# Performance work log

Measured on AMD Instinct MI355X. Metric: run time of the kernel, lower is better.

## Reference

```python
import jax, jax.numpy as jnp
import numpy as np

B, L, H, HEADS = 2, 2048, 1024, 16
D = H // HEADS  # head_dim = 64


def _rel_pos_bias(q, pos_emb):
    """Skewing trick: q is (b,h,L,d) (already scaled), pos_emb is (2L-1,d).
    Returns relative positional bias of shape (b,h,L,L)."""
    b, h, l, _ = q.shape
    p = jnp.einsum('bhid,jd->bhij', q, pos_emb)          # (b,h,L,2L-1)
    p = jnp.pad(p, ((0, 0), (0, 0), (0, 0), (0, 1)))     # (b,h,L,2L)
    p = p.reshape(b, h, l * 2 * l)                        # flatten last two dims
    p = jnp.pad(p, ((0, 0), (0, 0), (0, l - 1)))          # append L-1 zeros
    p = p.reshape(b, h, l + 1, 2 * l - 1)
    return p[:, :, :-1, -l:]                              # (b,h,L,L)


def setup_inputs() -> dict:
    key = jax.random.key(0)
    ks = jax.random.split(key, 12)
    s = 1.0 / np.sqrt(H)
    inp = {
        'query': jax.random.normal(ks[0], (B, L, H), jnp.float32),
        'key':   jax.random.normal(ks[1], (B, L, H), jnp.float32),
        'value': jax.random.normal(ks[2], (B, L, H), jnp.float32),
        'Wq_w': jax.random.normal(ks[3], (H, H), jnp.float32) * s,
        'Wq_b': jnp.zeros((H,), jnp.float32),
        'Wk_w': jax.random.normal(ks[4], (H, H), jnp.float32) * s,
        'Wk_b': jnp.zeros((H,), jnp.float32),
        'Wv_w': jax.random.normal(ks[5], (H, H), jnp.float32) * s,
        'Wv_b': jnp.zeros((H,), jnp.float32),
        'Wo_w': jax.random.normal(ks[6], (H, H), jnp.float32) * s,
        'Wo_b': jnp.zeros((H,), jnp.float32),
        'pos_emb': jax.random.normal(ks[7], (2 * L - 1, D), jnp.float32),
    }
    return inp


def reference(query, key, value, Wq_w, Wq_b, Wk_w, Wk_b, Wv_w, Wv_b, Wo_w, Wo_b, pos_emb):
    b = query.shape[0]
    q = query @ Wq_w.T + Wq_b
    k = key @ Wk_w.T + Wk_b
    v = value @ Wv_w.T + Wv_b
    # (b,L,h*d) -> (b,h,L,d)
    split = lambda x: x.reshape(b, L, HEADS, D).transpose(0, 2, 1, 3)
    q, k, v = split(q), split(k), split(v)
    q = q / np.sqrt(D)  # note: scaled q is also used for positional bias (faithful)
    attn = jnp.einsum('bhid,bhjd->bhij', q, k)
    attn = attn + _rel_pos_bias(q, pos_emb)
    causal = jnp.triu(jnp.full((L, L), -jnp.inf, jnp.float32), k=1)
    attn = attn + causal  # broadcasts over (b,h)
    score = jax.nn.softmax(attn, axis=-1)
    out = jnp.einsum('bhqk,bhkd->bhqd', score, v)
    out = out.transpose(0, 2, 1, 3).reshape(b, L, H)
    return out @ Wo_w.T + Wo_b
```

## Files before the change

### kernel.cpp

```cpp
#include <hip/hip_runtime.h>

#define L_SEQ 2048
#define NH    16
#define HD    64
#define HDIM  1024

typedef __attribute__((ext_vector_type(8))) short  short8;
typedef __attribute__((ext_vector_type(4))) float  f32x4;

__device__ __forceinline__ unsigned short f2bf(float f) {
    unsigned int u = __float_as_uint(f);
    u += 0x7fffu + ((u >> 16) & 1u);
    return (unsigned short)(u >> 16);
}

__device__ __forceinline__ short8 ld8(const unsigned short* p) {
    return *(const short8*)p;
}

__device__ __forceinline__ unsigned int cvtpk(float a, float b) {
    unsigned int r;
    asm("v_cvt_pk_bf16_f32 %0, %1, %2" : "=v"(r) : "v"(a), "v"(b));
    return r;
}

__device__ __forceinline__ void gl16(const unsigned short* g, unsigned short* l) {
    __builtin_amdgcn_global_load_lds(
        (const __attribute__((address_space(1))) void*)g,
        (__attribute__((address_space(3))) void*)l, 16, 0, 0);
}

__global__ __launch_bounds__(256) void cvt_x_kernel(const float* __restrict__ src,
                                                    unsigned short* __restrict__ dst) {
    const int i = blockIdx.x * 256 + threadIdx.x;
    const float4 a = ((const float4*)src)[2 * i];
    const float4 b = ((const float4*)src)[2 * i + 1];
    union { short8 v; unsigned int u[4]; } o;
    o.u[0] = cvtpk(a.x, a.y); o.u[1] = cvtpk(a.z, a.w);
    o.u[2] = cvtpk(b.x, b.y); o.u[3] = cvtpk(b.z, b.w);
    ((short8*)dst)[i] = o.v;
}

__global__ __launch_bounds__(256) void cvt_wpe_kernel(
    const float* __restrict__ Wq, const float* __restrict__ Wk,
    const float* __restrict__ Wv, const float* __restrict__ Wo,
    const float* __restrict__ pe,
    unsigned short* __restrict__ D, unsigned short* __restrict__ E) {
    const int y = blockIdx.y;
    const float* src = (y == 0) ? Wq : (y == 1) ? Wk : (y == 2) ? Wv : (y == 3) ? Wo : pe;
    unsigned short* dst = (y < 4) ? (D + (size_t)y * 1048576) : E;
    const int n8 = (y < 4) ? 131072 : 32760;
    const int i = blockIdx.x * 256 + threadIdx.x;
    if (i >= n8) return;
    const float4 a = ((const float4*)src)[2 * i];
    const float4 b = ((const float4*)src)[2 * i + 1];
    union { short8 v; unsigned int u[4]; } o;
    o.u[0] = cvtpk(a.x, a.y); o.u[1] = cvtpk(a.z, a.w);
    o.u[2] = cvtpk(b.x, b.y); o.u[3] = cvtpk(b.z, b.w);
    ((short8*)dst)[i] = o.v;
}

__device__ __forceinline__ void gemm_bf16_core(
    const unsigned short* __restrict__ Xb,
    const unsigned short* __restrict__ Wb,
    int row0, int col0,
    unsigned short* As, unsigned short* Bs,
    f32x4 (&acc)[4][4])
{
    const int t    = threadIdx.x;
    const int lane = t & 63;
    const int wid  = t >> 6;
    const int lr   = lane & 15;
    const int lg   = lane >> 4;
    const int wr   = (wid >> 1) << 6;
    const int wc   = (wid & 1) << 6;

    const int grow = lane >> 3;
    const int gcol = ((lane & 7) ^ grow) << 3;

#pragma unroll
    for (int m = 0; m < 4; ++m)
#pragma unroll
        for (int n = 0; n < 4; ++n)
            acc[m][n] = (f32x4)0.0f;

    const unsigned short* xs = Xb + (size_t)(row0 + grow) * 1024 + gcol;
    const unsigned short* ws = Wb + (size_t)(col0 + grow) * 1024 + gcol;

    for (int k0 = 0; k0 < 1024; k0 += 64) {
        __syncthreads();
#pragma unroll
        for (int i = 0; i < 4; ++i) {
            const int seg = (i << 2) + wid;
            gl16(xs + (size_t)(seg << 3) * 1024 + k0, As + seg * 512);
            gl16(ws + (size_t)(seg << 3) * 1024 + k0, Bs + seg * 512);
        }
        __syncthreads();

        short8 af[4][2], bf[4][2];
#pragma unroll
        for (int m = 0; m < 4; ++m) {
            const int row = wr + (m << 4) + lr;
#pragma unroll
            for (int h = 0; h < 2; ++h)
                af[m][h] = ld8(&As[row * 64 + ((((h << 2) + lg) ^ (lr & 7)) << 3)]);
        }
#pragma unroll
        for (int n = 0; n < 4; ++n) {
            const int row = wc + (n << 4) + lr;
#pragma unroll
            for (int h = 0; h < 2; ++h)
                bf[n][h] = ld8(&Bs[row * 64 + ((((h << 2) + lg) ^ (lr & 7)) << 3)]);
        }
#pragma unroll
        for (int m = 0; m < 4; ++m)
#pragma unroll
            for (int n = 0; n < 4; ++n) {
                acc[m][n] = __builtin_amdgcn_mfma_f32_16x16x32_bf16(af[m][0], bf[n][0], acc[m][n], 0, 0, 0);
                acc[m][n] = __builtin_amdgcn_mfma_f32_16x16x32_bf16(af[m][1], bf[n][1], acc[m][n], 0, 0, 0);
            }
    }
}

template<int MODE>
__global__ __launch_bounds__(256) void proj_kernel(
    const unsigned short* __restrict__ Xb, const unsigned short* __restrict__ Wb,
    const float* __restrict__ bias, unsigned short* __restrict__ out)
{
    __shared__ __align__(16) unsigned short As[128 * 64];
    __shared__ __align__(16) unsigned short Bs[128 * 64];

    const int d = blockIdx.x;
    const int y = ((d >> 6) << 3) | (d & 7);
    const int x = (d >> 3) & 7;
    const int row0 = y << 7, col0 = x << 7;

    f32x4 acc[4][4];
    gemm_bf16_core(Xb, Wb, row0, col0, As, Bs, acc);

    const int t = threadIdx.x;
    const int lane = t & 63;
    const int wid  = t >> 6;
    const int lr = lane & 15, lg = lane >> 4;
    const int wr = (wid >> 1) << 6, wc = (wid & 1) << 6;

    if (MODE <= 1) {
        const float scale = (MODE == 0) ? 0.125f : 1.0f;
#pragma unroll
        for (int n = 0; n < 4; ++n) {
            const int o = col0 + wc + (n << 4) + lr;
            const float bo = bias[o];
            const int h = o >> 6, dd = o & 63;
#pragma unroll
            for (int m = 0; m < 4; ++m) {
                const int ib = row0 + wr + (m << 4) + (lg << 2);
#pragma unroll
                for (int r = 0; r < 4; ++r) {
                    const int i = ib + r;
                    out[(((size_t)((i >> 11) * NH + h)) * L_SEQ + (i & (L_SEQ - 1))) * HD + dd] =
                        f2bf((acc[m][n][r] + bo) * scale);
                }
            }
        }
    } else {
#pragma unroll
        for (int n = 0; n < 4; ++n) {
            const int o = col0 + wc + (n << 4) + lr;
            const float bo = bias[o];
            const int h = o >> 6, dd = o & 63;
#pragma unroll
            for (int m = 0; m < 4; ++m) {
                const int ib = row0 + wr + (m << 4) + (lg << 2);
                const int b = ib >> 11, il = ib & (L_SEQ - 1);
                ushort4 pk;
                pk.x = f2bf(acc[m][n][0] + bo);
                pk.y = f2bf(acc[m][n][1] + bo);
                pk.z = f2bf(acc[m][n][2] + bo);
                pk.w = f2bf(acc[m][n][3] + bo);
                *(ushort4*)&out[(((size_t)(b * NH + h)) * HD + dd) * L_SEQ + il] = pk;
            }
        }
    }
}

__global__ __launch_bounds__(256) void outproj_kernel(
    const unsigned short* __restrict__ Ob, const unsigned short* __restrict__ Wb,
    const float* __restrict__ bias, float* __restrict__ Yout)
{
    __shared__ __align__(16) unsigned short As[128 * 64];
    __shared__ __align__(16) unsigned short Bs[128 * 64];

    const int d = blockIdx.x;
    const int y = ((d >> 6) << 3) | (d & 7);
    const int x = (d >> 3) & 7;
    const int row0 = y << 7, col0 = x << 7;

    f32x4 acc[4][4];
    gemm_bf16_core(Ob, Wb, row0, col0, As, Bs, acc);

    const int t = threadIdx.x;
    const int lane = t & 63;
    const int wid  = t >> 6;
    const int lr = lane & 15, lg = lane >> 4;
    const int wr = (wid >> 1) << 6, wc = (wid & 1) << 6;

#pragma unroll
    for (int n = 0; n < 4; ++n) {
        const int o = col0 + wc + (n << 4) + lr;
        const float bo = bias[o];
#pragma unroll
        for (int m = 0; m < 4; ++m) {
            const int ib = row0 + wr + (m << 4) + (lg << 2);
#pragma unroll
            for (int r = 0; r < 4; ++r)
                Yout[(size_t)(ib + r) * HDIM + o] = acc[m][n][r] + bo;
        }
    }
}

__global__ __launch_bounds__(256, 3) void attn_kernel(
    const unsigned short* __restrict__ Q,
    const unsigned short* __restrict__ Kt,
    const unsigned short* __restrict__ VT,
    const unsigned short* __restrict__ PE,
    unsigned short* __restrict__ O)
{
    __shared__ __align__(16) unsigned short Ks[2][64][64];
    __shared__ __align__(16) unsigned short Vs[2][64][64];
    __shared__ __align__(16) float blds_all[4][64][20];

    const int t    = threadIdx.x;
    const int wid  = t >> 6;
    const int lane = t & 63;
    const int lr   = lane & 15;
    const int lg   = lane >> 4;
    const int lk   = lg << 3;

    const int p   = blockIdx.x;
    const int bh  = p & 31;
    const int rb  = 31 - (p >> 5);
    const int i0  = rb << 6;
    const int i0w = i0 + (wid << 4);
    const int nt  = rb + 1;

    const unsigned short* kbase = Kt + (size_t)bh * L_SEQ * HD;
    const unsigned short* vbase = VT + (size_t)bh * HD * L_SEQ;

    const int srow = t >> 2;
    const int sc2  = (t & 3) << 1;
    const int swz  = srow & 7;

    short8 kstg[2], vstg[2];

    float (*blds)[20] = blds_all[wid];

    const unsigned short* qb = Q + ((size_t)bh * L_SEQ + i0w + lr) * HD + lk;
    const short8 aq0 = ld8(qb);
    const short8 aq1 = ld8(qb + 32);

    const int gi    = i0w + lr;
    const int idx0  = ((lg & 1) << 7) + (lr << 2);
    const int idx1  = idx0 + 64;
    const int selhi = lg >> 1;

    f32x4 oacc[4];
#pragma unroll
    for (int dt = 0; dt < 4; ++dt) oacc[dt] = (f32x4)0.0f;
    float mrun = -__builtin_inff();
    float lrun = 0.0f;

    const int jend = i0w + 15;

    f32x4 pqc = (f32x4)0.0f;
    {
        const unsigned short* pp = PE + (size_t)(2032 - i0w + lr) * HD + lk;
        pqc = __builtin_amdgcn_mfma_f32_16x16x32_bf16(aq0, ld8(pp), pqc, 0, 0, 0);
        pqc = __builtin_amdgcn_mfma_f32_16x16x32_bf16(aq1, ld8(pp + 32), pqc, 0, 0, 0);
    }

#pragma unroll
    for (int s = 0; s < 2; ++s) {
        kstg[s] = ld8(kbase + (size_t)srow * HD + ((sc2 + s) << 3));
        vstg[s] = ld8(vbase + (size_t)srow * L_SEQ + ((sc2 + s) << 3));
    }
#pragma unroll
    for (int s = 0; s < 2; ++s) {
        *(short8*)&Ks[0][srow][((sc2 + s) ^ swz) << 3] = kstg[s];
        *(short8*)&Vs[0][srow][((sc2 + s) ^ swz) << 3] = vstg[s];
    }
    __syncthreads();

    int cur = 0;
    for (int tt = 0; tt < nt; ++tt) {
        const int j0   = tt << 6;
        const bool more = (tt + 1 < nt);

        if (more) {
            const int jn = j0 + 64;
#pragma unroll
            for (int s = 0; s < 2; ++s) {
                kstg[s] = ld8(kbase + (size_t)(jn + srow) * HD + ((sc2 + s) << 3));
                vstg[s] = ld8(vbase + (size_t)srow * L_SEQ + jn + ((sc2 + s) << 3));
            }
        }

        if (j0 <= jend) {
            f32x4 s2[4];
#pragma unroll
            for (int ct = 0; ct < 4; ++ct) {
                const int row = (ct << 4) + lr;
                const short8 k0 = *(const short8*)&Ks[cur][row][(lg ^ (lr & 7)) << 3];
                const short8 k1 = *(const short8*)&Ks[cur][row][((4 + lg) ^ (lr & 7)) << 3];
                f32x4 a = (f32x4)0.0f;
                a = __builtin_amdgcn_mfma_f32_16x16x32_bf16(k0, aq0, a, 0, 0, 0);
                a = __builtin_amdgcn_mfma_f32_16x16x32_bf16(k1, aq1, a, 0, 0, 0);
                s2[ct] = a;
            }

            const int mlo = 2032 + j0 - i0w;
            f32x4 pq[5];
            pq[0] = pqc;
#pragma unroll
            for (int pt = 1; pt < 5; ++pt) {
                f32x4 a = (f32x4)0.0f;
                const unsigned short* pp = PE + (size_t)(mlo + (pt << 4) + lr) * HD + lk;
                a = __builtin_amdgcn_mfma_f32_16x16x32_bf16(aq0, ld8(pp), a, 0, 0, 0);
                a = __builtin_amdgcn_mfma_f32_16x16x32_bf16(aq1, ld8(pp + 32), a, 0, 0, 0);
                pq[pt] = a;
            }
            pqc = pq[4];

#pragma unroll
            for (int r = 0; r < 4; ++r) {
                const int qw = (lg << 2) + r;
                {
                    const int kr = lr + qw - 15;
                    if (kr >= 0) blds[kr][qw] = pq[0][r];
                }
#pragma unroll
                for (int pt = 1; pt < 4; ++pt)
                    blds[(pt << 4) + lr + qw - 15][qw] = pq[pt][r];
                {
                    const int kr = 49 + lr + qw;
                    if (kr < 64) blds[kr][qw] = pq[4][r];
                }
            }

#pragma unroll
            for (int ct = 0; ct < 4; ++ct)
#pragma unroll
                for (int r = 0; r < 4; ++r) {
                    const int krl = (ct << 4) + (lg << 2) + r;
                    const float v = s2[ct][r] + blds[krl][lr];
                    s2[ct][r] = (j0 + krl > gi) ? -__builtin_inff() : v;
                }

            float c0 = fmaxf(fmaxf(s2[0][0], s2[0][1]), fmaxf(s2[0][2], s2[0][3]));
            float c1 = fmaxf(fmaxf(s2[1][0], s2[1][1]), fmaxf(s2[1][2], s2[1][3]));
            float c2 = fmaxf(fmaxf(s2[2][0], s2[2][1]), fmaxf(s2[2][2], s2[2][3]));
            float c3 = fmaxf(fmaxf(s2[3][0], s2[3][1]), fmaxf(s2[3][2], s2[3][3]));
            float vmax = fmaxf(fmaxf(c0, c1), fmaxf(c2, c3));
            vmax = fmaxf(vmax, __shfl_xor(vmax, 16));
            vmax = fmaxf(vmax, __shfl_xor(vmax, 32));
            const float mnew = fmaxf(mrun, vmax);
            const float sc = __expf(mrun - mnew);
            mrun = mnew;
#pragma unroll
            for (int ct = 0; ct < 4; ++ct)
#pragma unroll
                for (int r = 0; r < 4; ++r)
                    s2[ct][r] = __expf(s2[ct][r] - mnew);
            float t0 = (s2[0][0] + s2[0][1]) + (s2[0][2] + s2[0][3]);
            float t1 = (s2[1][0] + s2[1][1]) + (s2[1][2] + s2[1][3]);
            float t2 = (s2[2][0] + s2[2][1]) + (s2[2][2] + s2[2][3]);
            float t3 = (s2[3][0] + s2[3][1]) + (s2[3][2] + s2[3][3]);
            float sum = (t0 + t1) + (t2 + t3);
            sum += __shfl_xor(sum, 16);
            sum += __shfl_xor(sum, 32);
            lrun = lrun * sc + sum;
#pragma unroll
            for (int dt = 0; dt < 4; ++dt)
#pragma unroll
                for (int r = 0; r < 4; ++r)
                    oacc[dt][r] *= sc;

            unsigned int pkl[4], pkh[4];
#pragma unroll
            for (int ct = 0; ct < 4; ++ct) {
                pkl[ct] = cvtpk(s2[ct][0], s2[ct][1]);
                pkh[ct] = cvtpk(s2[ct][2], s2[ct][3]);
            }
            union { short8 v; int u[4]; } pf0, pf1;
#pragma unroll
            for (int m = 0; m < 4; ++m) {
                const int bidx = (m & 2) ? idx1 : idx0;
                const int a0 = __builtin_amdgcn_ds_bpermute(bidx, (int)((m & 1) ? pkh[0] : pkl[0]));
                const int a1 = __builtin_amdgcn_ds_bpermute(bidx, (int)((m & 1) ? pkh[1] : pkl[1]));
                pf0.u[m] = selhi ? a1 : a0;
                const int b0 = __builtin_amdgcn_ds_bpermute(bidx, (int)((m & 1) ? pkh[2] : pkl[2]));
                const int b1 = __builtin_amdgcn_ds_bpermute(bidx, (int)((m & 1) ? pkh[3] : pkl[3]));
                pf1.u[m] = selhi ? b1 : b0;
            }

#pragma unroll
            for (int dt = 0; dt < 4; ++dt) {
                const int row = (dt << 4) + lr;
                const short8 v0 = *(const short8*)&Vs[cur][row][(lg ^ (lr & 7)) << 3];
                const short8 v1 = *(const short8*)&Vs[cur][row][((4 + lg) ^ (lr & 7)) << 3];
                oacc[dt] = __builtin_amdgcn_mfma_f32_16x16x32_bf16(v0, pf0.v, oacc[dt], 0, 0, 0);
                oacc[dt] = __builtin_amdgcn_mfma_f32_16x16x32_bf16(v1, pf1.v, oacc[dt], 0, 0, 0);
            }
        }

        if (more) {
#pragma unroll
            for (int s = 0; s < 2; ++s) {
                *(short8*)&Ks[cur ^ 1][srow][((sc2 + s) ^ swz) << 3] = kstg[s];
                *(short8*)&Vs[cur ^ 1][srow][((sc2 + s) ^ swz) << 3] = vstg[s];
            }
        }
        __syncthreads();
        cur ^= 1;
    }

    const float inv = 1.0f / lrun;
    const int b = bh >> 4, h = bh & 15;
#pragma unroll
    for (int dt = 0; dt < 4; ++dt) {
        uint2 u;
        u.x = cvtpk(oacc[dt][0] * inv, oacc[dt][1] * inv);
        u.y = cvtpk(oacc[dt][2] * inv, oacc[dt][3] * inv);
        *(uint2*)&O[((size_t)b * L_SEQ + i0w + lr) * HDIM + (h << 6) + (dt << 4) + (lg << 2)] = u;
    }
}

extern "C" void kernel_launch(void* const* d_in, const int* in_sizes, int n_in,
                              void* d_out, int out_size, void* d_ws, size_t ws_size,
                              hipStream_t stream) {
    (void)in_sizes; (void)n_in; (void)out_size;

    const float* query   = (const float*)d_in[0];
    const float* key_    = (const float*)d_in[1];
    const float* value   = (const float*)d_in[2];
    const float* Wq_w    = (const float*)d_in[3];
    const float* Wq_b    = (const float*)d_in[4];
    const float* Wk_w    = (const float*)d_in[5];
    const float* Wk_b    = (const float*)d_in[6];
    const float* Wv_w    = (const float*)d_in[7];
    const float* Wv_b    = (const float*)d_in[8];
    const float* Wo_w    = (const float*)d_in[9];
    const float* Wo_b    = (const float*)d_in[10];
    const float* pos_emb = (const float*)d_in[11];

    char* ws = (char*)d_ws;
    const size_t MB = 1024 * 1024;
    unsigned short* S1 = (unsigned short*)(ws);
    unsigned short* Qb = (unsigned short*)(ws + 8  * MB);
    unsigned short* Kb = (unsigned short*)(ws + 16 * MB);
    unsigned short* Vb = (unsigned short*)(ws + 24 * MB);
    unsigned short* D  = (unsigned short*)(ws + 32 * MB);
    unsigned short* E  = (unsigned short*)(ws + 40 * MB);

    const int npe = (2 * L_SEQ - 1) * HD;
    if (ws_size < (size_t)40 * MB + (size_t)npe * 2) return;

    cvt_wpe_kernel<<<dim3(512, 5), 256, 0, stream>>>(Wq_w, Wk_w, Wv_w, Wo_w, pos_emb, D, E);
    cvt_x_kernel<<<2048, 256, 0, stream>>>(query, S1);
    cvt_x_kernel<<<2048, 256, 0, stream>>>(key_, Vb);
    proj_kernel<0><<<256, 256, 0, stream>>>(S1, D, Wq_b, Qb);
    proj_kernel<1><<<256, 256, 0, stream>>>(Vb, D + 1048576, Wk_b, Kb);
    cvt_x_kernel<<<2048, 256, 0, stream>>>(value, S1);
    proj_kernel<2><<<256, 256, 0, stream>>>(S1, D + 2097152, Wv_b, Vb);
    attn_kernel<<<1024, 256, 0, stream>>>(Qb, Kb, Vb, E, S1);
    outproj_kernel<<<256, 256, 0, stream>>>(S1, D + 3145728, Wo_b, (float*)d_out);
}
```

Before: 203.1 us.

## Merge conversion and Q/K projection launches; stage K/V via direct global-to-LDS loads

```diff
diff --git a/kernel.cpp b/kernel.cpp
--- a/kernel.cpp
+++ b/kernel.cpp
@@ -28,6 +28,35 @@
     __builtin_amdgcn_global_load_lds(
         (const __attribute__((address_space(1))) void*)g,
         (__attribute__((address_space(3))) void*)l, 16, 0, 0);
+}
+
+__global__ __launch_bounds__(256) void cvt_a_kernel(
+    const float* __restrict__ q, const float* __restrict__ k,
+    const float* __restrict__ Wq, const float* __restrict__ Wk,
+    const float* __restrict__ Wv, const float* __restrict__ Wo,
+    const float* __restrict__ pe,
+    unsigned short* __restrict__ S1, unsigned short* __restrict__ Vb,
+    unsigned short* __restrict__ D, unsigned short* __restrict__ E)
+{
+    const int y = blockIdx.y;
+    const float* src; unsigned short* dst; int n8;
+    switch (y) {
+        case 0:  src = q;  dst = S1;            n8 = 524288; break;
+        case 1:  src = k;  dst = Vb;            n8 = 524288; break;
+        case 2:  src = Wq; dst = D;             n8 = 131072; break;
+        case 3:  src = Wk; dst = D + 1048576;   n8 = 131072; break;
+        case 4:  src = Wv; dst = D + 2097152;   n8 = 131072; break;
+        case 5:  src = Wo; dst = D + 3145728;   n8 = 131072; break;
+        default: src = pe; dst = E;             n8 = 32760;  break;
+    }
+    const int i = blockIdx.x * 256 + threadIdx.x;
+    if (i >= n8) return;
+    const float4 a = ((const float4*)src)[2 * i];
+    const float4 b = ((const float4*)src)[2 * i + 1];
+    union { short8 v; unsigned int u[4]; } o;
+    o.u[0] = cvtpk(a.x, a.y); o.u[1] = cvtpk(a.z, a.w);
+    o.u[2] = cvtpk(b.x, b.y); o.u[3] = cvtpk(b.z, b.w);
+    ((short8*)dst)[i] = o.v;
 }
 
 __global__ __launch_bounds__(256) void cvt_x_kernel(const float* __restrict__ src,
@@ -41,25 +70,6 @@
     ((short8*)dst)[i] = o.v;
 }
 
-__global__ __launch_bounds__(256) void cvt_wpe_kernel(
-    const float* __restrict__ Wq, const float* __restrict__ Wk,
-    const float* __restrict__ Wv, const float* __restrict__ Wo,
-    const float* __restrict__ pe,
-    unsigned short* __restrict__ D, unsigned short* __restrict__ E) {
-    const int y = blockIdx.y;
-    const float* src = (y == 0) ? Wq : (y == 1) ? Wk : (y == 2) ? Wv : (y == 3) ? Wo : pe;
-    unsigned short* dst = (y < 4) ? (D + (size_t)y * 1048576) : E;
-    const int n8 = (y < 4) ? 131072 : 32760;
-    const int i = blockIdx.x * 256 + threadIdx.x;
-    if (i >= n8) return;
-    const float4 a = ((const float4*)src)[2 * i];
-    const float4 b = ((const float4*)src)[2 * i + 1];
-    union { short8 v; unsigned int u[4]; } o;
-    o.u[0] = cvtpk(a.x, a.y); o.u[1] = cvtpk(a.z, a.w);
-    o.u[2] = cvtpk(b.x, b.y); o.u[3] = cvtpk(b.z, b.w);
-    ((short8*)dst)[i] = o.v;
-}
-
 __device__ __forceinline__ void gemm_bf16_core(
     const unsigned short* __restrict__ Xb,
     const unsigned short* __restrict__ Wb,
@@ -122,18 +132,26 @@
     }
 }
 
-template<int MODE>
-__global__ __launch_bounds__(256) void proj_kernel(
-    const unsigned short* __restrict__ Xb, const unsigned short* __restrict__ Wb,
-    const float* __restrict__ bias, unsigned short* __restrict__ out)
+__global__ __launch_bounds__(256) void proj_qk_kernel(
+    const unsigned short* __restrict__ Xq, const unsigned short* __restrict__ Xk,
+    const unsigned short* __restrict__ D,
+    const float* __restrict__ bq, const float* __restrict__ bk,
+    unsigned short* __restrict__ Qb, unsigned short* __restrict__ Kb)
 {
     __shared__ __align__(16) unsigned short As[128 * 64];
     __shared__ __align__(16) unsigned short Bs[128 * 64];
 
-    const int d = blockIdx.x;
+    const int z = blockIdx.x >> 8;
+    const int d = blockIdx.x & 255;
     const int y = ((d >> 6) << 3) | (d & 7);
     const int x = (d >> 3) & 7;
     const int row0 = y << 7, col0 = x << 7;
+
+    const unsigned short* Xb = z ? Xk : Xq;
+    const unsigned short* Wb = D + (z ? 1048576 : 0);
+    const float* bias = z ? bk : bq;
+    unsigned short* out = z ? Kb : Qb;
+    const float scale = z ? 1.0f : 0.125f;
 
     f32x4 acc[4][4];
     gemm_bf16_core(Xb, Wb, row0, col0, As, Bs, acc);
@@ -144,48 +162,27 @@
     const int lr = lane & 15, lg = lane >> 4;
     const int wr = (wid >> 1) << 6, wc = (wid & 1) << 6;
 
-    if (MODE <= 1) {
-        const float scale = (MODE == 0) ? 0.125f : 1.0f;
-#pragma unroll
-        for (int n = 0; n < 4; ++n) {
-            const int o = col0 + wc + (n << 4) + lr;
-            const float bo = bias[o];
-            const int h = o >> 6, dd = o & 63;
-#pragma unroll
-            for (int m = 0; m < 4; ++m) {
-                const int ib = row0 + wr + (m << 4) + (lg << 2);
-#pragma unroll
-                for (int r = 0; r < 4; ++r) {
-                    const int i = ib + r;
-                    out[(((size_t)((i >> 11) * NH + h)) * L_SEQ + (i & (L_SEQ - 1))) * HD + dd] =
-                        f2bf((acc[m][n][r] + bo) * scale);
-                }
-            }
-        }
-    } else {
-#pragma unroll
-        for (int n = 0; n < 4; ++n) {
-            const int o = col0 + wc + (n << 4) + lr;
-            const float bo = bias[o];
-            const int h = o >> 6, dd = o & 63;
-#pragma unroll
-            for (int m = 0; m < 4; ++m) {
-                const int ib = row0 + wr + (m << 4) + (lg << 2);
-                const int b = ib >> 11, il = ib & (L_SEQ - 1);
-                ushort4 pk;
-                pk.x = f2bf(acc[m][n][0] + bo);
-                pk.y = f2bf(acc[m][n][1] + bo);
-                pk.z = f2bf(acc[m][n][2] + bo);
-                pk.w = f2bf(acc[m][n][3] + bo);
-                *(ushort4*)&out[(((size_t)(b * NH + h)) * HD + dd) * L_SEQ + il] = pk;
-            }
-        }
-    }
-}
-
-__global__ __launch_bounds__(256) void outproj_kernel(
-    const unsigned short* __restrict__ Ob, const unsigned short* __restrict__ Wb,
-    const float* __restrict__ bias, float* __restrict__ Yout)
+#pragma unroll
+    for (int n = 0; n < 4; ++n) {
+        const int o = col0 + wc + (n << 4) + lr;
+        const float bo = bias[o];
+        const int h = o >> 6, dd = o & 63;
+#pragma unroll
+        for (int m = 0; m < 4; ++m) {
+            const int ib = row0 + wr + (m << 4) + (lg << 2);
+#pragma unroll
+            for (int r = 0; r < 4; ++r) {
+                const int i = ib + r;
+                out[(((size_t)((i >> 11) * NH + h)) * L_SEQ + (i & (L_SEQ - 1))) * HD + dd] =
+                    f2bf((acc[m][n][r] + bo) * scale);
+            }
+        }
+    }
+}
+
+__global__ __launch_bounds__(256) void proj_v_kernel(
+    const unsigned short* __restrict__ Xb, const unsigned short* __restrict__ Wb,
+    const float* __restrict__ bias, unsigned short* __restrict__ out)
 {
     __shared__ __align__(16) unsigned short As[128 * 64];
     __shared__ __align__(16) unsigned short Bs[128 * 64];
@@ -196,7 +193,7 @@
     const int row0 = y << 7, col0 = x << 7;
 
     f32x4 acc[4][4];
-    gemm_bf16_core(Ob, Wb, row0, col0, As, Bs, acc);
+    gemm_bf16_core(Xb, Wb, row0, col0, As, Bs, acc);
 
     const int t = threadIdx.x;
     const int lane = t & 63;
@@ -208,13 +205,67 @@
     for (int n = 0; n < 4; ++n) {
         const int o = col0 + wc + (n << 4) + lr;
         const float bo = bias[o];
+        const int h = o >> 6, dd = o & 63;
 #pragma unroll
         for (int m = 0; m < 4; ++m) {
             const int ib = row0 + wr + (m << 4) + (lg << 2);
+            const int b = ib >> 11, il = ib & (L_SEQ - 1);
+            ushort4 pk;
+            pk.x = f2bf(acc[m][n][0] + bo);
+            pk.y = f2bf(acc[m][n][1] + bo);
+            pk.z = f2bf(acc[m][n][2] + bo);
+            pk.w = f2bf(acc[m][n][3] + bo);
+            *(ushort4*)&out[(((size_t)(b * NH + h)) * HD + dd) * L_SEQ + il] = pk;
+        }
+    }
+}
+
+__global__ __launch_bounds__(256) void outproj_kernel(
+    const unsigned short* __restrict__ Ob, const unsigned short* __restrict__ Wb,
+    const float* __restrict__ bias, float* __restrict__ Yout)
+{
+    __shared__ __align__(16) unsigned short As[128 * 64];
+    __shared__ __align__(16) unsigned short Bs[128 * 64];
+
+    const int d = blockIdx.x;
+    const int y = ((d >> 6) << 3) | (d & 7);
+    const int x = (d >> 3) & 7;
+    const int row0 = y << 7, col0 = x << 7;
+
+    f32x4 acc[4][4];
+    gemm_bf16_core(Ob, Wb, row0, col0, As, Bs, acc);
+
+    const int t = threadIdx.x;
+    const int lane = t & 63;
+    const int wid  = t >> 6;
+    const int lr = lane & 15, lg = lane >> 4;
+    const int wr = (wid >> 1) << 6, wc = (wid & 1) << 6;
+
+#pragma unroll
+    for (int n = 0; n < 4; ++n) {
+        const int o = col0 + wc + (n << 4) + lr;
+        const float bo = bias[o];
+#pragma unroll
+        for (int m = 0; m < 4; ++m) {
+            const int ib = row0 + wr + (m << 4) + (lg << 2);
 #pragma unroll
             for (int r = 0; r < 4; ++r)
                 Yout[(size_t)(ib + r) * HDIM + o] = acc[m][n][r] + bo;
         }
+    }
+}
+
+__device__ __forceinline__ void stage_kv(
+    const unsigned short* __restrict__ kbase, const unsigned short* __restrict__ vbase,
+    int j0, unsigned short (*Ksb)[64], unsigned short (*Vsb)[64], int wid, int lane)
+{
+    const int r8 = lane >> 3;
+    const int gc = ((lane & 7) ^ r8) << 3;
+#pragma unroll
+    for (int s = 0; s < 2; ++s) {
+        const int rw = (wid << 4) + (s << 3);
+        gl16(kbase + (size_t)(j0 + rw + r8) * HD + gc, &Ksb[rw][0]);
+        gl16(vbase + (size_t)(rw + r8) * L_SEQ + j0 + gc, &Vsb[rw][0]);
     }
 }
 
@@ -246,12 +297,6 @@
     const unsigned short* kbase = Kt + (size_t)bh * L_SEQ * HD;
     const unsigned short* vbase = VT + (size_t)bh * HD * L_SEQ;
 
-    const int srow = t >> 2;
-    const int sc2  = (t & 3) << 1;
-    const int swz  = srow & 7;
-
-    short8 kstg[2], vstg[2];
-
     float (*blds)[20] = blds_all[wid];
 
     const unsigned short* qb = Q + ((size_t)bh * L_SEQ + i0w + lr) * HD + lk;
@@ -278,16 +323,7 @@
         pqc = __builtin_amdgcn_mfma_f32_16x16x32_bf16(aq1, ld8(pp + 32), pqc, 0, 0, 0);
     }
 
-#pragma unroll
-    for (int s = 0; s < 2; ++s) {
-        kstg[s] = ld8(kbase + (size_t)srow * HD + ((sc2 + s) << 3));
-        vstg[s] = ld8(vbase + (size_t)srow * L_SEQ + ((sc2 + s) << 3));
-    }
-#pragma unroll
-    for (int s = 0; s < 2; ++s) {
-        *(short8*)&Ks[0][srow][((sc2 + s) ^ swz) << 3] = kstg[s];
-        *(short8*)&Vs[0][srow][((sc2 + s) ^ swz) << 3] = vstg[s];
-    }
+    stage_kv(kbase, vbase, 0, Ks[0], Vs[0], wid, lane);
     __syncthreads();
 
     int cur = 0;
@@ -295,14 +331,8 @@
         const int j0   = tt << 6;
         const bool more = (tt + 1 < nt);
 
-        if (more) {
-            const int jn = j0 + 64;
-#pragma unroll
-            for (int s = 0; s < 2; ++s) {
-                kstg[s] = ld8(kbase + (size_t)(jn + srow) * HD + ((sc2 + s) << 3));
-                vstg[s] = ld8(vbase + (size_t)srow * L_SEQ + jn + ((sc2 + s) << 3));
-            }
-        }
+        if (more)
+            stage_kv(kbase, vbase, j0 + 64, Ks[cur ^ 1], Vs[cur ^ 1], wid, lane);
 
         if (j0 <= jend) {
             f32x4 s2[4];
@@ -412,13 +442,6 @@
             }
         }
 
-        if (more) {
-#pragma unroll
-            for (int s = 0; s < 2; ++s) {
-                *(short8*)&Ks[cur ^ 1][srow][((sc2 + s) ^ swz) << 3] = kstg[s];
-                *(short8*)&Vs[cur ^ 1][srow][((sc2 + s) ^ swz) << 3] = vstg[s];
-            }
-        }
         __syncthreads();
         cur ^= 1;
     }
@@ -464,13 +487,11 @@
     const int npe = (2 * L_SEQ - 1) * HD;
     if (ws_size < (size_t)40 * MB + (size_t)npe * 2) return;
 
-    cvt_wpe_kernel<<<dim3(512, 5), 256, 0, stream>>>(Wq_w, Wk_w, Wv_w, Wo_w, pos_emb, D, E);
-    cvt_x_kernel<<<2048, 256, 0, stream>>>(query, S1);
-    cvt_x_kernel<<<2048, 256, 0, stream>>>(key_, Vb);
-    proj_kernel<0><<<256, 256, 0, stream>>>(S1, D, Wq_b, Qb);
-    proj_kernel<1><<<256, 256, 0, stream>>>(Vb, D + 1048576, Wk_b, Kb);
+    cvt_a_kernel<<<dim3(2048, 7), 256, 0, stream>>>(query, key_, Wq_w, Wk_w, Wv_w, Wo_w,
+                                                    pos_emb, S1, Vb, D, E);
+    proj_qk_kernel<<<512, 256, 0, stream>>>(S1, Vb, D, Wq_b, Wk_b, Qb, Kb);
     cvt_x_kernel<<<2048, 256, 0, stream>>>(value, S1);
-    proj_kernel<2><<<256, 256, 0, stream>>>(S1, D + 2097152, Wv_b, Vb);
+    proj_v_kernel<<<256, 256, 0, stream>>>(S1, D + 2097152, Wv_b, Vb);
     attn_kernel<<<1024, 256, 0, stream>>>(Qb, Kb, Vb, E, S1);
     outproj_kernel<<<256, 256, 0, stream>>>(S1, D + 3145728, Wo_b, (float*)d_out);
 }
```

After: 179.5 us. 1.13x faster.
